# Kernel optimization log

Hardware: AMD Instinct MI355X
Metric: run time of the kernel (lower is better)

## Reference

```python
import jax, jax.numpy as jnp
import numpy as np

EMBED_DIM = 1024
NUM_HEADS = 16
HEAD_DIM = EMBED_DIM // NUM_HEADS


def setup_inputs() -> dict:
    key = jax.random.key(0)
    ks = jax.random.split(key, 11)
    L, N, E = 2048, 2, EMBED_DIM
    S = 2048
    def xavier(k, shape):
        fan_in, fan_out = shape[1], shape[0]
        limit = float(np.sqrt(6.0 / (fan_in + fan_out)))
        return jax.random.uniform(k, shape, jnp.float32, -limit, limit)
    return {
        "query": jax.random.normal(ks[0], (L, N, E), jnp.float32),
        "key": jax.random.normal(ks[1], (S, N, E), jnp.float32),
        "value": jax.random.normal(ks[2], (S, N, E), jnp.float32),
        "Wq": xavier(ks[3], (E, E)), "bq": jnp.zeros((E,), jnp.float32),
        "Wk": xavier(ks[4], (E, E)), "bk": jnp.zeros((E,), jnp.float32),
        "Wv": xavier(ks[5], (E, E)), "bv": jnp.zeros((E,), jnp.float32),
        "Wo": xavier(ks[6], (E, E)), "bo": jnp.zeros((E,), jnp.float32),
    }


def reference(query, key, value, Wq, bq, Wk, bk, Wv, bv, Wo, bo):
    # query/key/value: [L, N, E] (seq-first, batch_first=False)
    L, N, E = query.shape
    S = key.shape[0]
    H, D = NUM_HEADS, HEAD_DIM
    q = query @ Wq.T + bq   # [L, N, E]
    k = key @ Wk.T + bk     # [S, N, E]
    v = value @ Wv.T + bv   # [S, N, E]
    # [L, N*H, D] -> [N*H, L, D]
    q = q.reshape(L, N * H, D).transpose(1, 0, 2)
    k = k.reshape(S, N * H, D).transpose(1, 0, 2)
    v = v.reshape(S, N * H, D).transpose(1, 0, 2)
    scores = jnp.einsum("bld,bsd->bls", q, k) / jnp.sqrt(jnp.float32(D))  # [N*H, L, S]
    attn = jax.nn.softmax(scores, axis=-1)  # dropout p=0.0 -> identity
    out = jnp.einsum("bls,bsd->bld", attn, v)  # [N*H, L, D]
    out = out.transpose(1, 0, 2).reshape(L, N, E)
    attn_output = out @ Wo.T + bo  # [L, N, E]
    # need_weights=True, average_attn_weights=True
    attn_weights = attn.reshape(N, H, L, S).mean(axis=1)  # [N, L, S]
    return attn_output, attn_weights
```

## Files before the change

kernel.cpp:

```cpp
#include <hip/hip_runtime.h>

#define EDIM 1024
#define LSEQ 2048
#define NBATCH 2
#define NHEADS 16
#define HDIM 64
#define QSCALE 0.18033688011112042f

typedef unsigned short us;
typedef __attribute__((ext_vector_type(8))) short short8;
typedef __attribute__((ext_vector_type(4))) float floatx4;
typedef __attribute__((ext_vector_type(16))) float floatx16;

#define MFMA16(a, b, c) __builtin_amdgcn_mfma_f32_16x16x32_bf16((a), (b), (c), 0, 0, 0)
#define MFMA32(a, b, c) __builtin_amdgcn_mfma_f32_32x32x16_bf16((a), (b), (c), 0, 0, 0)
#define ZERO16 ((floatx16){0.f,0.f,0.f,0.f,0.f,0.f,0.f,0.f,0.f,0.f,0.f,0.f,0.f,0.f,0.f,0.f})

#define WAIT_VM8 asm volatile("s_waitcnt vmcnt(8)" ::: "memory")
#define WAIT_VM4 asm volatile("s_waitcnt vmcnt(4)" ::: "memory")
#define WAIT_VM0 asm volatile("s_waitcnt vmcnt(0)" ::: "memory")
#define WAIT_LGKM0 asm volatile("s_waitcnt lgkmcnt(0)" ::: "memory")
#define CFENCE asm volatile("" ::: "memory")

__device__ __forceinline__ us f2bf(float f) {
  unsigned int u = __float_as_uint(f);
  u += 0x7fffu + ((u >> 16) & 1u);
  return (us)(u >> 16);
}

__device__ __forceinline__ void gload16(const void* g, void* l) {
  __builtin_amdgcn_global_load_lds((const __attribute__((address_space(1))) unsigned int*)g,
                                   (__attribute__((address_space(3))) unsigned int*)l, 16, 0, 0);
}

__device__ __forceinline__ unsigned int cvtpk(float lo, float hi_) {
  unsigned int r;
  asm("v_cvt_pk_bf16_f32 %0, %1, %2" : "=v"(r) : "v"(lo), "v"(hi_));
  return r;
}
__device__ __forceinline__ void plswap(unsigned int& a, unsigned int& b) {
  asm("v_permlane32_swap_b32 %0, %1" : "+v"(a), "+v"(b));
}
__device__ __forceinline__ short8 mkfrag(unsigned int a, unsigned int b, unsigned int c,
                                         unsigned int d) {
  union { unsigned int u[4]; short8 v; } x;
  x.u[0] = a; x.u[1] = b; x.u[2] = c; x.u[3] = d;
  return x.v;
}
__device__ __forceinline__ void pack2(const floatx16 p, short8& f0, short8& f1) {
  unsigned int A = cvtpk(p[0], p[1]), B = cvtpk(p[4], p[5]); plswap(A, B);
  unsigned int C = cvtpk(p[2], p[3]), D = cvtpk(p[6], p[7]); plswap(C, D);
  f0 = mkfrag(A, C, B, D);
  unsigned int E = cvtpk(p[8], p[9]), F = cvtpk(p[12], p[13]); plswap(E, F);
  unsigned int G = cvtpk(p[10], p[11]), H = cvtpk(p[14], p[15]); plswap(G, H);
  f1 = mkfrag(E, G, F, H);
}

__global__ void k_f2bf_all(const float* q, const float* k, const float* v,
                           const float* wq, const float* wk, const float* wv, const float* wo,
                           us* dq, us* dk, us* dv, us* dwq, us* dwk, us* dwv, us* dwo) {
  const int z = blockIdx.y;
  const float* s; us* d; int n8;
  if (z == 0)      { s = q;  d = dq;  n8 = 524288; }
  else if (z == 1) { s = k;  d = dk;  n8 = 524288; }
  else if (z == 2) { s = v;  d = dv;  n8 = 524288; }
  else if (z == 3) { s = wq; d = dwq; n8 = 131072; }
  else if (z == 4) { s = wk; d = dwk; n8 = 131072; }
  else if (z == 5) { s = wv; d = dwv; n8 = 131072; }
  else             { s = wo; d = dwo; n8 = 131072; }
  int i = blockIdx.x * blockDim.x + threadIdx.x;
  int stride = gridDim.x * blockDim.x;
  for (; i < n8; i += stride) {
    float4 a = ((const float4*)s)[2 * i];
    float4 b = ((const float4*)s)[2 * i + 1];
    union { us u[8]; uint4 vv; } o;
    o.u[0] = f2bf(a.x); o.u[1] = f2bf(a.y); o.u[2] = f2bf(a.z); o.u[3] = f2bf(a.w);
    o.u[4] = f2bf(b.x); o.u[5] = f2bf(b.y); o.u[6] = f2bf(b.z); o.u[7] = f2bf(b.w);
    ((uint4*)d)[i] = o.vv;
  }
}

template <int MODE>
__device__ __forceinline__ void gemm_core(us* pool,
                                          const us* __restrict__ A, const us* __restrict__ B,
                                          const float* __restrict__ bias, void* __restrict__ outp,
                                          int row0, int col0, float scale) {
  const int t = threadIdx.x;
  const int w = t >> 6, lane = t & 63;
  const int g = lane >> 4, lr = lane & 15;
  const int wm = (w & 1) * 64, wn = (w >> 1) * 64;
  const int srow = lane >> 2, scol = (lane & 3) * 8;
  const int cA = 2 * w;
  const us* Asrc = A + (size_t)(row0 + cA * 16 + srow) * EDIM + scol;
  const us* Bsrc = B + (size_t)(col0 + cA * 16 + srow) * EDIM + scol;

  floatx4 acc[4][4];
#pragma unroll
  for (int mi = 0; mi < 4; ++mi)
#pragma unroll
    for (int ni = 0; ni < 4; ++ni) acc[mi][ni] = (floatx4){0.f, 0.f, 0.f, 0.f};

  auto stage = [&](int kt, us* Ab) {
    const int k0 = kt * 32;
    us* Bb = Ab + 4096;
    gload16(Asrc + k0, Ab + cA * 512);
    gload16(Asrc + 16 * EDIM + k0, Ab + cA * 512 + 512);
    gload16(Bsrc + k0, Bb + cA * 512);
    gload16(Bsrc + 16 * EDIM + k0, Bb + cA * 512 + 512);
  };

  stage(0, pool);
  stage(1, pool + 8192);

  int cur = 0, nxt = 2;
  for (int kt = 0; kt < 32; ++kt) {
    if (kt < 31) { WAIT_VM4; } else { WAIT_VM0; }
    __builtin_amdgcn_s_barrier();
    CFENCE;
    if (kt + 2 < 32) {
      stage(kt + 2, pool + nxt * 8192);
      nxt = (nxt == 2) ? 0 : nxt + 1;
    }
    const us* Ac = pool + cur * 8192;
    const us* Bc = Ac + 4096;
    short8 af[4], bfr[4];
#pragma unroll
    for (int mi = 0; mi < 4; ++mi) af[mi] = *(const short8*)&Ac[(wm + mi * 16 + lr) * 32 + g * 8];
#pragma unroll
    for (int ni = 0; ni < 4; ++ni) bfr[ni] = *(const short8*)&Bc[(wn + ni * 16 + lr) * 32 + g * 8];
#pragma unroll
    for (int mi = 0; mi < 4; ++mi)
#pragma unroll
      for (int ni = 0; ni < 4; ++ni) acc[mi][ni] = MFMA16(af[mi], bfr[ni], acc[mi][ni]);
    WAIT_LGKM0;
    CFENCE;
    cur = (cur == 2) ? 0 : cur + 1;
  }

  if (MODE == 1) {
    __syncthreads();
    us* Ct = pool;
#pragma unroll
    for (int ni = 0; ni < 4; ++ni) {
      const int colloc = wn + ni * 16 + lr;
      const float bv = bias[col0 + colloc];
#pragma unroll
      for (int mi = 0; mi < 4; ++mi) {
        const int b = wm + mi * 16 + 4 * g;
        unsigned int lo = (unsigned int)f2bf(acc[mi][ni][0] + bv) |
                          ((unsigned int)f2bf(acc[mi][ni][2] + bv) << 16);
        unsigned int hi = (unsigned int)f2bf(acc[mi][ni][1] + bv) |
                          ((unsigned int)f2bf(acc[mi][ni][3] + bv) << 16);
        *(unsigned int*)&Ct[colloc * 136 + (b >> 1)] = lo;
        *(unsigned int*)&Ct[colloc * 136 + 64 + (b >> 1)] = hi;
      }
    }
    __syncthreads();
    const int rr = t >> 1, half = t & 1;
    const int c = col0 + rr, h = c >> 6, d = c & 63;
    us* dst = (us*)outp + (((size_t)half * NHEADS + h) * HDIM + d) * LSEQ + (row0 >> 1);
    const us* srcRow = &Ct[rr * 136 + half * 64];
#pragma unroll
    for (int j = 0; j < 8; ++j)
      *(uint4*)(dst + j * 8) = *(const uint4*)(srcRow + j * 8);
  } else {
#pragma unroll
    for (int ni = 0; ni < 4; ++ni) {
      const int col = col0 + wn + ni * 16 + lr;
      const float bv = bias[col];
#pragma unroll
      for (int mi = 0; mi < 4; ++mi) {
#pragma unroll
        for (int i = 0; i < 4; ++i) {
          const int row = row0 + wm + mi * 16 + g * 4 + i;
          const float v = (acc[mi][ni][i] + bv) * scale;
          if (MODE == 2) {
            ((float*)outp)[(size_t)row * EDIM + col] = v;
          } else {
            const int n = row & 1, sq = row >> 1;
            const int h = col >> 6, d = col & 63;
            ((us*)outp)[(((size_t)n * NHEADS + h) * LSEQ + sq) * HDIM + d] = f2bf(v);
          }
        }
      }
    }
  }
}

__global__ __launch_bounds__(256) void k_gemm_qkv(
    const us* __restrict__ Xq, const us* __restrict__ Xk, const us* __restrict__ Xv,
    const us* __restrict__ Wqb, const us* __restrict__ Wkb, const us* __restrict__ Wvb,
    const float* __restrict__ bq, const float* __restrict__ bk, const float* __restrict__ bv,
    us* __restrict__ qo, us* __restrict__ ko, us* __restrict__ vo) {
  __shared__ us pool[24576];
  const int z = blockIdx.z;
  if (z == 0)      gemm_core<0>(pool, Xq, Wqb, bq, qo, blockIdx.x * 128, blockIdx.y * 128, QSCALE);
  else if (z == 1) gemm_core<0>(pool, Xk, Wkb, bk, ko, blockIdx.x * 128, blockIdx.y * 128, 1.0f);
  else             gemm_core<1>(pool, Xv, Wvb, bv, vo, blockIdx.x * 128, blockIdx.y * 128, 1.0f);
}

__global__ __launch_bounds__(256) void k_gemm_o(const us* __restrict__ A, const us* __restrict__ B,
                                                const float* __restrict__ bias, float* __restrict__ out) {
  __shared__ us pool[24576];
  gemm_core<2>(pool, A, B, bias, out, blockIdx.x * 128, blockIdx.y * 128, 1.0f);
}

__global__ __launch_bounds__(256) void k_attn(const us* __restrict__ qb, const us* __restrict__ kb,
                                              const us* __restrict__ vt, float* __restrict__ rell,
                                              us* __restrict__ O) {
  __shared__ us Ks[4][4096];
  __shared__ us Vs[4][4096];
  __shared__ float elt[4][32];
  const int bh = blockIdx.x;
  const int l0 = blockIdx.y * 128;
  const int t = threadIdx.x, w = t >> 6, lane = t & 63;
  const int ql = lane & 31, hi = lane >> 5;
  const int lbase = l0 + w * 32;

  short8 qf[4];
  {
    const us* qptr = qb + ((size_t)bh * LSEQ + lbase + ql) * HDIM + hi * 8;
#pragma unroll
    for (int dt = 0; dt < 4; ++dt) qf[dt] = *(const short8*)(qptr + dt * 16);
  }

  int off0[4], off1[4];
#pragma unroll
  for (int j = 0; j < 4; ++j) {
    off0[j] = ql * 64 + (((2 * j + hi) ^ (ql & 7)) << 3);
    off1[j] = (32 + ql) * 64 + (((2 * j + hi) ^ (ql & 7)) << 3);
  }

  const int j0 = 2 * w, j1 = 2 * w + 1;
  const int srA = lane >> 3;
  const int scA = ((lane & 7) ^ (lane >> 3)) * 8;
  const us* Kbase = kb + (size_t)bh * LSEQ * HDIM;
  const us* Vbase = vt + (size_t)bh * HDIM * LSEQ;
  const us* Ksrc0 = Kbase + (j0 * 8 + srA) * HDIM + scA;
  const us* Ksrc1 = Kbase + (j1 * 8 + srA) * HDIM + scA;
  const us* Vsrc0 = Vbase + (size_t)(j0 * 8 + srA) * LSEQ + scA;
  const us* Vsrc1 = Vbase + (size_t)(j1 * 8 + srA) * LSEQ + scA;

  floatx16 oacc0 = ZERO16, oacc1 = ZERO16;
  float ellacc = 0.f;

  auto stageKV = [&](int kt, int b) {
    const int so = kt * 64;
    gload16(Ksrc0 + so * HDIM, &Ks[b][j0 * 512]);
    gload16(Ksrc1 + so * HDIM, &Ks[b][j1 * 512]);
    gload16(Vsrc0 + so, &Vs[b][j0 * 512]);
    gload16(Vsrc1 + so, &Vs[b][j1 * 512]);
  };

  stageKV(0, 0);
  stageKV(1, 1);
  stageKV(2, 2);

  for (int it = 0; it < 32; ++it) {
    if (it < 30) { WAIT_VM8; } else if (it == 30) { WAIT_VM4; } else { WAIT_VM0; }
    __builtin_amdgcn_s_barrier();
    CFENCE;
    if (it + 3 < 32) stageKV(it + 3, (it + 3) & 3);
    const us* Kc = Ks[it & 3];
    const us* Vc = Vs[it & 3];

    floatx16 acc0 = ZERO16, acc1 = ZERO16;
    __builtin_amdgcn_s_setprio(1);
#pragma unroll
    for (int dt = 0; dt < 4; ++dt) {
      acc0 = MFMA32(*(const short8*)&Kc[off0[dt]], qf[dt], acc0);
      acc1 = MFMA32(*(const short8*)&Kc[off1[dt]], qf[dt], acc1);
    }
    __builtin_amdgcn_s_setprio(0);
#pragma unroll
    for (int r = 0; r < 16; ++r) {
      acc0[r] = __builtin_amdgcn_exp2f(acc0[r]); ellacc += acc0[r];
      acc1[r] = __builtin_amdgcn_exp2f(acc1[r]); ellacc += acc1[r];
    }
    short8 pa0, pa1, pa2, pa3;
    pack2(acc0, pa0, pa1);
    pack2(acc1, pa2, pa3);
    __builtin_amdgcn_s_setprio(1);
#pragma unroll
    for (int dt2 = 0; dt2 < 2; ++dt2) {
      floatx16& oa = dt2 ? oacc1 : oacc0;
      const int* off = dt2 ? off1 : off0;
      oa = MFMA32(pa0, *(const short8*)&Vc[off[0]], oa);
      oa = MFMA32(pa1, *(const short8*)&Vc[off[1]], oa);
      oa = MFMA32(pa2, *(const short8*)&Vc[off[2]], oa);
      oa = MFMA32(pa3, *(const short8*)&Vc[off[3]], oa);
    }
    __builtin_amdgcn_s_setprio(0);
  }

  const float elltot = ellacc + __shfl_xor(ellacc, 32);
  if (lane < 32) {
    const float r0 = 1.0f / elltot;
    elt[w][lane] = r0;
    rell[(size_t)bh * LSEQ + lbase + lane] = r0;
  }
  const int n = bh >> 4, hh = bh & 15;
  us* obase = O + (size_t)n * EDIM + (size_t)hh * HDIM;
#pragma unroll
  for (int r = 0; r < 16; ++r) {
    const int q = (r & 3) + 8 * (r >> 2) + 4 * hi;
    const float rl = elt[w][q];
    const size_t l = lbase + q;
    obase[l * (NBATCH * EDIM) + ql] = f2bf(oacc0[r] * rl);
    obase[l * (NBATCH * EDIM) + 32 + ql] = f2bf(oacc1[r] * rl);
  }
}

__global__ __launch_bounds__(256, 2) void k_weights(const us* __restrict__ qb, const us* __restrict__ kb,
                                                    const float* __restrict__ rell,
                                                    float* __restrict__ Wout) {
  __shared__ us Ks[2][4096];
  const int l0 = blockIdx.x * 256;
  const int s0 = blockIdx.y * 64;
  const int n = blockIdx.z;
  const int t = threadIdx.x, w = t >> 6, lane = t & 63;
  const int ql = lane & 31, hi = lane >> 5;
  const int lbase = l0 + w * 64;
  const int j0 = 2 * w, j1 = 2 * w + 1;
  const int srA = lane >> 3;
  const int scA = ((lane & 7) ^ (lane >> 3)) * 8;
  const us* Kb0 = kb + ((size_t)(n * NHEADS) * LSEQ + s0 + j0 * 8 + srA) * HDIM + scA;
  const us* Kb1 = kb + ((size_t)(n * NHEADS) * LSEQ + s0 + j1 * 8 + srA) * HDIM + scA;

  int off0[4], off1[4];
#pragma unroll
  for (int j = 0; j < 4; ++j) {
    off0[j] = ql * 64 + (((2 * j + hi) ^ (ql & 7)) << 3);
    off1[j] = (32 + ql) * 64 + (((2 * j + hi) ^ (ql & 7)) << 3);
  }

  floatx16 wa00 = ZERO16, wa01 = ZERO16, wa10 = ZERO16, wa11 = ZERO16;

  gload16(Kb0, &Ks[0][j0 * 512]); gload16(Kb1, &Ks[0][j1 * 512]);

  short8 qc0[4], qc1[4];
  float rlc0, rlc1;
  {
    const us* qp0 = qb + ((size_t)(n * NHEADS) * LSEQ + lbase + ql) * HDIM + hi * 8;
    const us* qp1 = qp0 + 32 * HDIM;
#pragma unroll
    for (int dt = 0; dt < 4; ++dt) {
      qc0[dt] = *(const short8*)(qp0 + dt * 16);
      qc1[dt] = *(const short8*)(qp1 + dt * 16);
    }
    rlc0 = rell[(size_t)(n * NHEADS) * LSEQ + lbase + ql];
    rlc1 = rell[(size_t)(n * NHEADS) * LSEQ + lbase + 32 + ql];
  }
  __syncthreads();

  for (int h = 0; h < NHEADS; ++h) {
    const int cur = h & 1;
    short8 qn0[4], qn1[4];
    float rln0 = 0.f, rln1 = 0.f;
    if (h < NHEADS - 1) {
      us* Kn2 = Ks[cur ^ 1];
      gload16(Kb0 + (size_t)(h + 1) * LSEQ * HDIM, Kn2 + j0 * 512);
      gload16(Kb1 + (size_t)(h + 1) * LSEQ * HDIM, Kn2 + j1 * 512);
      const us* qp0 = qb + ((size_t)(n * NHEADS + h + 1) * LSEQ + lbase + ql) * HDIM + hi * 8;
      const us* qp1 = qp0 + 32 * HDIM;
#pragma unroll
      for (int dt = 0; dt < 4; ++dt) {
        qn0[dt] = *(const short8*)(qp0 + dt * 16);
        qn1[dt] = *(const short8*)(qp1 + dt * 16);
      }
      rln0 = rell[(size_t)(n * NHEADS + h + 1) * LSEQ + lbase + ql];
      rln1 = rell[(size_t)(n * NHEADS + h + 1) * LSEQ + lbase + 32 + ql];
    }
    const us* Kc = Ks[cur];
    short8 kf0[4], kf1[4];
#pragma unroll
    for (int dt = 0; dt < 4; ++dt) {
      kf0[dt] = *(const short8*)&Kc[off0[dt]];
      kf1[dt] = *(const short8*)&Kc[off1[dt]];
    }
    {
      floatx16 aA = ZERO16, aB = ZERO16;
#pragma unroll
      for (int dt = 0; dt < 4; ++dt) {
        aA = MFMA32(kf0[dt], qc0[dt], aA);
        aB = MFMA32(kf1[dt], qc0[dt], aB);
      }
#pragma unroll
      for (int r = 0; r < 16; ++r) {
        wa00[r] += __builtin_amdgcn_exp2f(aA[r]) * rlc0;
        wa01[r] += __builtin_amdgcn_exp2f(aB[r]) * rlc0;
      }
    }
    {
      floatx16 cA = ZERO16, cB = ZERO16;
#pragma unroll
      for (int dt = 0; dt < 4; ++dt) {
        cA = MFMA32(kf0[dt], qc1[dt], cA);
        cB = MFMA32(kf1[dt], qc1[dt], cB);
      }
#pragma unroll
      for (int r = 0; r < 16; ++r) {
        wa10[r] += __builtin_amdgcn_exp2f(cA[r]) * rlc1;
        wa11[r] += __builtin_amdgcn_exp2f(cB[r]) * rlc1;
      }
    }
#pragma unroll
    for (int dt = 0; dt < 4; ++dt) { qc0[dt] = qn0[dt]; qc1[dt] = qn1[dt]; }
    rlc0 = rln0; rlc1 = rln1;
    __syncthreads();
  }

  float* wb0 = Wout + (size_t)n * LSEQ * LSEQ + (size_t)(lbase + ql) * LSEQ + s0;
  float* wb1 = Wout + (size_t)n * LSEQ * LSEQ + (size_t)(lbase + 32 + ql) * LSEQ + s0;
#pragma unroll
  for (int r = 0; r < 16; ++r) {
    const int cr = (r & 3) + 8 * (r >> 2) + 4 * hi;
    wb0[cr] = wa00[r] * 0.0625f;
    wb0[32 + cr] = wa01[r] * 0.0625f;
    wb1[cr] = wa10[r] * 0.0625f;
    wb1[32 + cr] = wa11[r] * 0.0625f;
  }
}

extern "C" void kernel_launch(void* const* d_in, const int* in_sizes, int n_in,
                              void* d_out, int out_size, void* d_ws, size_t ws_size,
                              hipStream_t stream) {
  const float* query = (const float*)d_in[0];
  const float* key   = (const float*)d_in[1];
  const float* value = (const float*)d_in[2];
  const float* Wq = (const float*)d_in[3]; const float* bq = (const float*)d_in[4];
  const float* Wk = (const float*)d_in[5]; const float* bk = (const float*)d_in[6];
  const float* Wv = (const float*)d_in[7]; const float* bv = (const float*)d_in[8];
  const float* Wo = (const float*)d_in[9]; const float* bo = (const float*)d_in[10];

  const size_t MB = 1u << 20;
  char* ws = (char*)d_ws;
  us* Xq  = (us*)(ws + 0 * MB);
  us* Xk  = (us*)(ws + 8 * MB);
  us* Xv  = (us*)(ws + 16 * MB);
  us* Wqb = (us*)(ws + 24 * MB);
  us* Wkb = (us*)(ws + 26 * MB);
  us* Wvb = (us*)(ws + 28 * MB);
  us* Wob = (us*)(ws + 30 * MB);
  us* qbuf = (us*)(ws + 32 * MB);
  us* kbuf = (us*)(ws + 40 * MB);
  us* Vt   = (us*)(ws + 48 * MB);
  us* Obuf = (us*)(ws + 56 * MB);
  float* rell = (float*)(ws + 64 * MB);

  k_f2bf_all<<<dim3(256, 7), 256, 0, stream>>>(query, key, value, Wq, Wk, Wv, Wo,
                                               Xq, Xk, Xv, Wqb, Wkb, Wvb, Wob);

  k_gemm_qkv<<<dim3(32, 8, 3), 256, 0, stream>>>(Xq, Xk, Xv, Wqb, Wkb, Wvb, bq, bk, bv,
                                                 qbuf, kbuf, Vt);

  k_attn<<<dim3(32, 16), 256, 0, stream>>>(qbuf, kbuf, Vt, rell, Obuf);

  k_gemm_o<<<dim3(32, 8), 256, 0, stream>>>(Obuf, Wob, bo, (float*)d_out);
  k_weights<<<dim3(8, 32, 2), 256, 0, stream>>>(qbuf, kbuf, rell, (float*)d_out + 4194304);
}
```

Measured before the change: 156.7 us.

## Merge output projection GEMM and attention-weights kernels into one interleaved launch

Combines the output-projection GEMM (256 blocks) and the averaged attention-weights kernel (512 blocks) into a single 768-block launch. Block ids are interleaved so every third block runs the GEMM and the rest compute weights. The aim is to remove one launch and the tail idle time between the two kernels, letting the independent pieces of work fill the device together. In exchange the GEMM now runs under launch_bounds(256,2) with the larger shared pool, which may constrain its registers or occupancy.

```diff
diff --git a/kernel.cpp b/kernel.cpp
--- a/kernel.cpp
+++ b/kernel.cpp
@@ -199,10 +199,132 @@
   else             gemm_core<1>(pool, Xv, Wvb, bv, vo, blockIdx.x * 128, blockIdx.y * 128, 1.0f);
 }
 
-__global__ __launch_bounds__(256) void k_gemm_o(const us* __restrict__ A, const us* __restrict__ B,
-                                                const float* __restrict__ bias, float* __restrict__ out) {
+__device__ __forceinline__ void weights_core(us* poolraw, const us* __restrict__ qb,
+                                             const us* __restrict__ kb,
+                                             const float* __restrict__ rell,
+                                             float* __restrict__ Wout,
+                                             int l0, int s0, int n) {
+  us (*Ks)[4096] = (us(*)[4096])poolraw;
+  const int t = threadIdx.x, w = t >> 6, lane = t & 63;
+  const int ql = lane & 31, hi = lane >> 5;
+  const int lbase = l0 + w * 64;
+  const int j0 = 2 * w, j1 = 2 * w + 1;
+  const int srA = lane >> 3;
+  const int scA = ((lane & 7) ^ (lane >> 3)) * 8;
+  const us* Kb0 = kb + ((size_t)(n * NHEADS) * LSEQ + s0 + j0 * 8 + srA) * HDIM + scA;
+  const us* Kb1 = kb + ((size_t)(n * NHEADS) * LSEQ + s0 + j1 * 8 + srA) * HDIM + scA;
+
+  int off0[4], off1[4];
+#pragma unroll
+  for (int j = 0; j < 4; ++j) {
+    off0[j] = ql * 64 + (((2 * j + hi) ^ (ql & 7)) << 3);
+    off1[j] = (32 + ql) * 64 + (((2 * j + hi) ^ (ql & 7)) << 3);
+  }
+
+  floatx16 wa00 = ZERO16, wa01 = ZERO16, wa10 = ZERO16, wa11 = ZERO16;
+
+  gload16(Kb0, &Ks[0][j0 * 512]); gload16(Kb1, &Ks[0][j1 * 512]);
+
+  short8 qc0[4], qc1[4];
+  float rlc0, rlc1;
+  {
+    const us* qp0 = qb + ((size_t)(n * NHEADS) * LSEQ + lbase + ql) * HDIM + hi * 8;
+    const us* qp1 = qp0 + 32 * HDIM;
+#pragma unroll
+    for (int dt = 0; dt < 4; ++dt) {
+      qc0[dt] = *(const short8*)(qp0 + dt * 16);
+      qc1[dt] = *(const short8*)(qp1 + dt * 16);
+    }
+    rlc0 = rell[(size_t)(n * NHEADS) * LSEQ + lbase + ql];
+    rlc1 = rell[(size_t)(n * NHEADS) * LSEQ + lbase + 32 + ql];
+  }
+  __syncthreads();
+
+  for (int h = 0; h < NHEADS; ++h) {
+    const int cur = h & 1;
+    short8 qn0[4], qn1[4];
+    float rln0 = 0.f, rln1 = 0.f;
+    if (h < NHEADS - 1) {
+      us* Kn2 = Ks[cur ^ 1];
+      gload16(Kb0 + (size_t)(h + 1) * LSEQ * HDIM, Kn2 + j0 * 512);
+      gload16(Kb1 + (size_t)(h + 1) * LSEQ * HDIM, Kn2 + j1 * 512);
+      const us* qp0 = qb + ((size_t)(n * NHEADS + h + 1) * LSEQ + lbase + ql) * HDIM + hi * 8;
+      const us* qp1 = qp0 + 32 * HDIM;
+#pragma unroll
+      for (int dt = 0; dt < 4; ++dt) {
+        qn0[dt] = *(const short8*)(qp0 + dt * 16);
+        qn1[dt] = *(const short8*)(qp1 + dt * 16);
+      }
+      rln0 = rell[(size_t)(n * NHEADS + h + 1) * LSEQ + lbase + ql];
+      rln1 = rell[(size_t)(n * NHEADS + h + 1) * LSEQ + lbase + 32 + ql];
+    }
+    const us* Kc = Ks[cur];
+    short8 kf0[4], kf1[4];
+#pragma unroll
+    for (int dt = 0; dt < 4; ++dt) {
+      kf0[dt] = *(const short8*)&Kc[off0[dt]];
+      kf1[dt] = *(const short8*)&Kc[off1[dt]];
+    }
+    {
+      floatx16 aA = ZERO16, aB = ZERO16;
+#pragma unroll
+      for (int dt = 0; dt < 4; ++dt) {
+        aA = MFMA32(kf0[dt], qc0[dt], aA);
+        aB = MFMA32(kf1[dt], qc0[dt], aB);
+      }
+#pragma unroll
+      for (int r = 0; r < 16; ++r) {
+        wa00[r] += __builtin_amdgcn_exp2f(aA[r]) * rlc0;
+        wa01[r] += __builtin_amdgcn_exp2f(aB[r]) * rlc0;
+      }
+    }
+    {
+      floatx16 cA = ZERO16, cB = ZERO16;
+#pragma unroll
+      for (int dt = 0; dt < 4; ++dt) {
+        cA = MFMA32(kf0[dt], qc1[dt], cA);
+        cB = MFMA32(kf1[dt], qc1[dt], cB);
+      }
+#pragma unroll
+      for (int r = 0; r < 16; ++r) {
+        wa10[r] += __builtin_amdgcn_exp2f(cA[r]) * rlc1;
+        wa11[r] += __builtin_amdgcn_exp2f(cB[r]) * rlc1;
+      }
+    }
+#pragma unroll
+    for (int dt = 0; dt < 4; ++dt) { qc0[dt] = qn0[dt]; qc1[dt] = qn1[dt]; }
+    rlc0 = rln0; rlc1 = rln1;
+    __syncthreads();
+  }
+
+  float* wb0 = Wout + (size_t)n * LSEQ * LSEQ + (size_t)(lbase + ql) * LSEQ + s0;
+  float* wb1 = Wout + (size_t)n * LSEQ * LSEQ + (size_t)(lbase + 32 + ql) * LSEQ + s0;
+#pragma unroll
+  for (int r = 0; r < 16; ++r) {
+    const int cr = (r & 3) + 8 * (r >> 2) + 4 * hi;
+    wb0[cr] = wa00[r] * 0.0625f;
+    wb0[32 + cr] = wa01[r] * 0.0625f;
+    wb1[cr] = wa10[r] * 0.0625f;
+    wb1[32 + cr] = wa11[r] * 0.0625f;
+  }
+}
+
+__global__ __launch_bounds__(256, 2) void k_tail(
+    const us* __restrict__ Obuf, const us* __restrict__ Wob, const float* __restrict__ bo,
+    float* __restrict__ out, const us* __restrict__ qb, const us* __restrict__ kb,
+    const float* __restrict__ rell, float* __restrict__ Wout) {
   __shared__ us pool[24576];
-  gemm_core<2>(pool, A, B, bias, out, blockIdx.x * 128, blockIdx.y * 128, 1.0f);
+  const int id = blockIdx.x;
+  if (id % 3 == 0) {
+    const int gid = id / 3;
+    gemm_core<2>(pool, Obuf, Wob, bo, out, (gid & 31) * 128, (gid >> 5) * 128, 1.0f);
+  } else {
+    const int wid = id - id / 3 - 1;
+    const int l0 = (wid & 7) * 256;
+    const int s0 = ((wid >> 3) & 31) * 64;
+    const int n = wid >> 8;
+    weights_core(pool, qb, kb, rell, Wout, l0, s0, n);
+  }
 }
 
 __global__ __launch_bounds__(256) void k_attn(const us* __restrict__ qb, const us* __restrict__ kb,
@@ -308,117 +430,6 @@
     const size_t l = lbase + q;
     obase[l * (NBATCH * EDIM) + ql] = f2bf(oacc0[r] * rl);
     obase[l * (NBATCH * EDIM) + 32 + ql] = f2bf(oacc1[r] * rl);
-  }
-}
-
-__global__ __launch_bounds__(256, 2) void k_weights(const us* __restrict__ qb, const us* __restrict__ kb,
-                                                    const float* __restrict__ rell,
-                                                    float* __restrict__ Wout) {
-  __shared__ us Ks[2][4096];
-  const int l0 = blockIdx.x * 256;
-  const int s0 = blockIdx.y * 64;
-  const int n = blockIdx.z;
-  const int t = threadIdx.x, w = t >> 6, lane = t & 63;
-  const int ql = lane & 31, hi = lane >> 5;
-  const int lbase = l0 + w * 64;
-  const int j0 = 2 * w, j1 = 2 * w + 1;
-  const int srA = lane >> 3;
-  const int scA = ((lane & 7) ^ (lane >> 3)) * 8;
-  const us* Kb0 = kb + ((size_t)(n * NHEADS) * LSEQ + s0 + j0 * 8 + srA) * HDIM + scA;
-  const us* Kb1 = kb + ((size_t)(n * NHEADS) * LSEQ + s0 + j1 * 8 + srA) * HDIM + scA;
-
-  int off0[4], off1[4];
-#pragma unroll
-  for (int j = 0; j < 4; ++j) {
-    off0[j] = ql * 64 + (((2 * j + hi) ^ (ql & 7)) << 3);
-    off1[j] = (32 + ql) * 64 + (((2 * j + hi) ^ (ql & 7)) << 3);
-  }
-
-  floatx16 wa00 = ZERO16, wa01 = ZERO16, wa10 = ZERO16, wa11 = ZERO16;
-
-  gload16(Kb0, &Ks[0][j0 * 512]); gload16(Kb1, &Ks[0][j1 * 512]);
-
-  short8 qc0[4], qc1[4];
-  float rlc0, rlc1;
-  {
-    const us* qp0 = qb + ((size_t)(n * NHEADS) * LSEQ + lbase + ql) * HDIM + hi * 8;
-    const us* qp1 = qp0 + 32 * HDIM;
-#pragma unroll
-    for (int dt = 0; dt < 4; ++dt) {
-      qc0[dt] = *(const short8*)(qp0 + dt * 16);
-      qc1[dt] = *(const short8*)(qp1 + dt * 16);
-    }
-    rlc0 = rell[(size_t)(n * NHEADS) * LSEQ + lbase + ql];
-    rlc1 = rell[(size_t)(n * NHEADS) * LSEQ + lbase + 32 + ql];
-  }
-  __syncthreads();
-
-  for (int h = 0; h < NHEADS; ++h) {
-    const int cur = h & 1;
-    short8 qn0[4], qn1[4];
-    float rln0 = 0.f, rln1 = 0.f;
-    if (h < NHEADS - 1) {
-      us* Kn2 = Ks[cur ^ 1];
-      gload16(Kb0 + (size_t)(h + 1) * LSEQ * HDIM, Kn2 + j0 * 512);
-      gload16(Kb1 + (size_t)(h + 1) * LSEQ * HDIM, Kn2 + j1 * 512);
-      const us* qp0 = qb + ((size_t)(n * NHEADS + h + 1) * LSEQ + lbase + ql) * HDIM + hi * 8;
-      const us* qp1 = qp0 + 32 * HDIM;
-#pragma unroll
-      for (int dt = 0; dt < 4; ++dt) {
-        qn0[dt] = *(const short8*)(qp0 + dt * 16);
-        qn1[dt] = *(const short8*)(qp1 + dt * 16);
-      }
-      rln0 = rell[(size_t)(n * NHEADS + h + 1) * LSEQ + lbase + ql];
-      rln1 = rell[(size_t)(n * NHEADS + h + 1) * LSEQ + lbase + 32 + ql];
-    }
-    const us* Kc = Ks[cur];
-    short8 kf0[4], kf1[4];
-#pragma unroll
-    for (int dt = 0; dt < 4; ++dt) {
-      kf0[dt] = *(const short8*)&Kc[off0[dt]];
-      kf1[dt] = *(const short8*)&Kc[off1[dt]];
-    }
-    {
-      floatx16 aA = ZERO16, aB = ZERO16;
-#pragma unroll
-      for (int dt = 0; dt < 4; ++dt) {
-        aA = MFMA32(kf0[dt], qc0[dt], aA);
-        aB = MFMA32(kf1[dt], qc0[dt], aB);
-      }
-#pragma unroll
-      for (int r = 0; r < 16; ++r) {
-        wa00[r] += __builtin_amdgcn_exp2f(aA[r]) * rlc0;
-        wa01[r] += __builtin_amdgcn_exp2f(aB[r]) * rlc0;
-      }
-    }
-    {
-      floatx16 cA = ZERO16, cB = ZERO16;
-#pragma unroll
-      for (int dt = 0; dt < 4; ++dt) {
-        cA = MFMA32(kf0[dt], qc1[dt], cA);
-        cB = MFMA32(kf1[dt], qc1[dt], cB);
-      }
-#pragma unroll
-      for (int r = 0; r < 16; ++r) {
-        wa10[r] += __builtin_amdgcn_exp2f(cA[r]) * rlc1;
-        wa11[r] += __builtin_amdgcn_exp2f(cB[r]) * rlc1;
-      }
-    }
-#pragma unroll
-    for (int dt = 0; dt < 4; ++dt) { qc0[dt] = qn0[dt]; qc1[dt] = qn1[dt]; }
-    rlc0 = rln0; rlc1 = rln1;
-    __syncthreads();
-  }
-
-  float* wb0 = Wout + (size_t)n * LSEQ * LSEQ + (size_t)(lbase + ql) * LSEQ + s0;
-  float* wb1 = Wout + (size_t)n * LSEQ * LSEQ + (size_t)(lbase + 32 + ql) * LSEQ + s0;
-#pragma unroll
-  for (int r = 0; r < 16; ++r) {
-    const int cr = (r & 3) + 8 * (r >> 2) + 4 * hi;
-    wb0[cr] = wa00[r] * 0.0625f;
-    wb0[32 + cr] = wa01[r] * 0.0625f;
-    wb1[cr] = wa10[r] * 0.0625f;
-    wb1[32 + cr] = wa11[r] * 0.0625f;
   }
 }
 
@@ -456,6 +467,6 @@
 
   k_attn<<<dim3(32, 16), 256, 0, stream>>>(qbuf, kbuf, Vt, rell, Obuf);
 
-  k_gemm_o<<<dim3(32, 8), 256, 0, stream>>>(Obuf, Wob, bo, (float*)d_out);
-  k_weights<<<dim3(8, 32, 2), 256, 0, stream>>>(qbuf, kbuf, rell, (float*)d_out + 4194304);
-}
+  k_tail<<<dim3(768), 256, 0, stream>>>(Obuf, Wob, bo, (float*)d_out,
+                                        qbuf, kbuf, rell, (float*)d_out + 4194304);
+}
```

Measured after the change: 166.5 us. 6.3% more time.

## Give each attention wave 64 query rows to reuse K/V fragments across two tiles

Applied to the files above, without the earlier changes.

The attention kernel now runs 2 waves of 128 threads per block instead of 4. Each wave handles 64 query rows as two 32-row tiles that share the K and V fragments loaded from LDS, and each thread issues twice as many async global-to-LDS loads, with the vmcnt waits adjusted to match. This halves the LDS reads of K/V per unit of MFMA work and gives each wave more independent MFMA chains. In exchange it raises register pressure from four output accumulators and fewer waves per block, which may lower occupancy and latency hiding.

```diff
diff --git a/kernel.cpp b/kernel.cpp
--- a/kernel.cpp
+++ b/kernel.cpp
@@ -16,6 +16,7 @@
 #define MFMA32(a, b, c) __builtin_amdgcn_mfma_f32_32x32x16_bf16((a), (b), (c), 0, 0, 0)
 #define ZERO16 ((floatx16){0.f,0.f,0.f,0.f,0.f,0.f,0.f,0.f,0.f,0.f,0.f,0.f,0.f,0.f,0.f,0.f})
 
+#define WAIT_VM16 asm volatile("s_waitcnt vmcnt(16)" ::: "memory")
 #define WAIT_VM8 asm volatile("s_waitcnt vmcnt(8)" ::: "memory")
 #define WAIT_VM4 asm volatile("s_waitcnt vmcnt(4)" ::: "memory")
 #define WAIT_VM0 asm volatile("s_waitcnt vmcnt(0)" ::: "memory")
@@ -205,23 +206,27 @@
   gemm_core<2>(pool, A, B, bias, out, blockIdx.x * 128, blockIdx.y * 128, 1.0f);
 }
 
-__global__ __launch_bounds__(256) void k_attn(const us* __restrict__ qb, const us* __restrict__ kb,
+__global__ __launch_bounds__(128) void k_attn(const us* __restrict__ qb, const us* __restrict__ kb,
                                               const us* __restrict__ vt, float* __restrict__ rell,
                                               us* __restrict__ O) {
   __shared__ us Ks[4][4096];
   __shared__ us Vs[4][4096];
-  __shared__ float elt[4][32];
+  __shared__ float elt[2][64];
   const int bh = blockIdx.x;
   const int l0 = blockIdx.y * 128;
   const int t = threadIdx.x, w = t >> 6, lane = t & 63;
   const int ql = lane & 31, hi = lane >> 5;
-  const int lbase = l0 + w * 32;
-
-  short8 qf[4];
+  const int lbase = l0 + w * 64;
+
+  short8 qfA[4], qfB[4];
   {
-    const us* qptr = qb + ((size_t)bh * LSEQ + lbase + ql) * HDIM + hi * 8;
-#pragma unroll
-    for (int dt = 0; dt < 4; ++dt) qf[dt] = *(const short8*)(qptr + dt * 16);
+    const us* qpA = qb + ((size_t)bh * LSEQ + lbase + ql) * HDIM + hi * 8;
+    const us* qpB = qpA + 32 * HDIM;
+#pragma unroll
+    for (int dt = 0; dt < 4; ++dt) {
+      qfA[dt] = *(const short8*)(qpA + dt * 16);
+      qfB[dt] = *(const short8*)(qpB + dt * 16);
+    }
   }
 
   int off0[4], off1[4];
@@ -231,25 +236,29 @@
     off1[j] = (32 + ql) * 64 + (((2 * j + hi) ^ (ql & 7)) << 3);
   }
 
-  const int j0 = 2 * w, j1 = 2 * w + 1;
   const int srA = lane >> 3;
   const int scA = ((lane & 7) ^ (lane >> 3)) * 8;
   const us* Kbase = kb + (size_t)bh * LSEQ * HDIM;
   const us* Vbase = vt + (size_t)bh * HDIM * LSEQ;
-  const us* Ksrc0 = Kbase + (j0 * 8 + srA) * HDIM + scA;
-  const us* Ksrc1 = Kbase + (j1 * 8 + srA) * HDIM + scA;
-  const us* Vsrc0 = Vbase + (size_t)(j0 * 8 + srA) * LSEQ + scA;
-  const us* Vsrc1 = Vbase + (size_t)(j1 * 8 + srA) * LSEQ + scA;
-
-  floatx16 oacc0 = ZERO16, oacc1 = ZERO16;
-  float ellacc = 0.f;
+  const us* Ksrc[4];
+  const us* Vsrc[4];
+#pragma unroll
+  for (int i = 0; i < 4; ++i) {
+    const int jj = 4 * w + i;
+    Ksrc[i] = Kbase + (jj * 8 + srA) * HDIM + scA;
+    Vsrc[i] = Vbase + (size_t)(jj * 8 + srA) * LSEQ + scA;
+  }
+
+  floatx16 oaA0 = ZERO16, oaA1 = ZERO16, oaB0 = ZERO16, oaB1 = ZERO16;
+  float ellA = 0.f, ellB = 0.f;
 
   auto stageKV = [&](int kt, int b) {
     const int so = kt * 64;
-    gload16(Ksrc0 + so * HDIM, &Ks[b][j0 * 512]);
-    gload16(Ksrc1 + so * HDIM, &Ks[b][j1 * 512]);
-    gload16(Vsrc0 + so, &Vs[b][j0 * 512]);
-    gload16(Vsrc1 + so, &Vs[b][j1 * 512]);
+#pragma unroll
+    for (int i = 0; i < 4; ++i) {
+      gload16(Ksrc[i] + so * HDIM, &Ks[b][(4 * w + i) * 512]);
+      gload16(Vsrc[i] + so, &Vs[b][(4 * w + i) * 512]);
+    }
   };
 
   stageKV(0, 0);
@@ -257,57 +266,94 @@
   stageKV(2, 2);
 
   for (int it = 0; it < 32; ++it) {
-    if (it < 30) { WAIT_VM8; } else if (it == 30) { WAIT_VM4; } else { WAIT_VM0; }
+    if (it < 30) { WAIT_VM16; } else if (it == 30) { WAIT_VM8; } else { WAIT_VM0; }
     __builtin_amdgcn_s_barrier();
     CFENCE;
     if (it + 3 < 32) stageKV(it + 3, (it + 3) & 3);
     const us* Kc = Ks[it & 3];
     const us* Vc = Vs[it & 3];
 
-    floatx16 acc0 = ZERO16, acc1 = ZERO16;
+    short8 kf0[4], kf1[4];
+#pragma unroll
+    for (int dt = 0; dt < 4; ++dt) {
+      kf0[dt] = *(const short8*)&Kc[off0[dt]];
+      kf1[dt] = *(const short8*)&Kc[off1[dt]];
+    }
+    short8 paA[4];
+    {
+      floatx16 a0 = ZERO16, a1 = ZERO16;
+      __builtin_amdgcn_s_setprio(1);
+#pragma unroll
+      for (int dt = 0; dt < 4; ++dt) {
+        a0 = MFMA32(kf0[dt], qfA[dt], a0);
+        a1 = MFMA32(kf1[dt], qfA[dt], a1);
+      }
+      __builtin_amdgcn_s_setprio(0);
+#pragma unroll
+      for (int r = 0; r < 16; ++r) {
+        a0[r] = __builtin_amdgcn_exp2f(a0[r]); ellA += a0[r];
+        a1[r] = __builtin_amdgcn_exp2f(a1[r]); ellA += a1[r];
+      }
+      pack2(a0, paA[0], paA[1]);
+      pack2(a1, paA[2], paA[3]);
+    }
+    short8 paB[4];
+    {
+      floatx16 c0 = ZERO16, c1 = ZERO16;
+      __builtin_amdgcn_s_setprio(1);
+#pragma unroll
+      for (int dt = 0; dt < 4; ++dt) {
+        c0 = MFMA32(kf0[dt], qfB[dt], c0);
+        c1 = MFMA32(kf1[dt], qfB[dt], c1);
+      }
+      __builtin_amdgcn_s_setprio(0);
+#pragma unroll
+      for (int r = 0; r < 16; ++r) {
+        c0[r] = __builtin_amdgcn_exp2f(c0[r]); ellB += c0[r];
+        c1[r] = __builtin_amdgcn_exp2f(c1[r]); ellB += c1[r];
+      }
+      pack2(c0, paB[0], paB[1]);
+      pack2(c1, paB[2], paB[3]);
+    }
     __builtin_amdgcn_s_setprio(1);
 #pragma unroll
-    for (int dt = 0; dt < 4; ++dt) {
-      acc0 = MFMA32(*(const short8*)&Kc[off0[dt]], qf[dt], acc0);
-      acc1 = MFMA32(*(const short8*)&Kc[off1[dt]], qf[dt], acc1);
+    for (int j = 0; j < 4; ++j) {
+      const short8 vf0 = *(const short8*)&Vc[off0[j]];
+      const short8 vf1 = *(const short8*)&Vc[off1[j]];
+      oaA0 = MFMA32(paA[j], vf0, oaA0);
+      oaA1 = MFMA32(paA[j], vf1, oaA1);
+      oaB0 = MFMA32(paB[j], vf0, oaB0);
+      oaB1 = MFMA32(paB[j], vf1, oaB1);
     }
     __builtin_amdgcn_s_setprio(0);
-#pragma unroll
-    for (int r = 0; r < 16; ++r) {
-      acc0[r] = __builtin_amdgcn_exp2f(acc0[r]); ellacc += acc0[r];
-      acc1[r] = __builtin_amdgcn_exp2f(acc1[r]); ellacc += acc1[r];
-    }
-    short8 pa0, pa1, pa2, pa3;
-    pack2(acc0, pa0, pa1);
-    pack2(acc1, pa2, pa3);
-    __builtin_amdgcn_s_setprio(1);
-#pragma unroll
-    for (int dt2 = 0; dt2 < 2; ++dt2) {
-      floatx16& oa = dt2 ? oacc1 : oacc0;
-      const int* off = dt2 ? off1 : off0;
-      oa = MFMA32(pa0, *(const short8*)&Vc[off[0]], oa);
-      oa = MFMA32(pa1, *(const short8*)&Vc[off[1]], oa);
-      oa = MFMA32(pa2, *(const short8*)&Vc[off[2]], oa);
-      oa = MFMA32(pa3, *(const short8*)&Vc[off[3]], oa);
-    }
-    __builtin_amdgcn_s_setprio(0);
-  }
-
-  const float elltot = ellacc + __shfl_xor(ellacc, 32);
+  }
+
+  const float eA = ellA + __shfl_xor(ellA, 32);
+  const float eB = ellB + __shfl_xor(ellB, 32);
   if (lane < 32) {
-    const float r0 = 1.0f / elltot;
-    elt[w][lane] = r0;
-    rell[(size_t)bh * LSEQ + lbase + lane] = r0;
+    const float rA = 1.0f / eA, rB = 1.0f / eB;
+    elt[w][lane] = rA;
+    elt[w][32 + lane] = rB;
+    rell[(size_t)bh * LSEQ + lbase + lane] = rA;
+    rell[(size_t)bh * LSEQ + lbase + 32 + lane] = rB;
   }
   const int n = bh >> 4, hh = bh & 15;
   us* obase = O + (size_t)n * EDIM + (size_t)hh * HDIM;
 #pragma unroll
   for (int r = 0; r < 16; ++r) {
     const int q = (r & 3) + 8 * (r >> 2) + 4 * hi;
-    const float rl = elt[w][q];
-    const size_t l = lbase + q;
-    obase[l * (NBATCH * EDIM) + ql] = f2bf(oacc0[r] * rl);
-    obase[l * (NBATCH * EDIM) + 32 + ql] = f2bf(oacc1[r] * rl);
+    {
+      const float rl = elt[w][q];
+      const size_t l = lbase + q;
+      obase[l * (NBATCH * EDIM) + ql] = f2bf(oaA0[r] * rl);
+      obase[l * (NBATCH * EDIM) + 32 + ql] = f2bf(oaA1[r] * rl);
+    }
+    {
+      const float rl = elt[w][32 + q];
+      const size_t l = lbase + 32 + q;
+      obase[l * (NBATCH * EDIM) + ql] = f2bf(oaB0[r] * rl);
+      obase[l * (NBATCH * EDIM) + 32 + ql] = f2bf(oaB1[r] * rl);
+    }
   }
 }
 
@@ -454,7 +500,7 @@
   k_gemm_qkv<<<dim3(32, 8, 3), 256, 0, stream>>>(Xq, Xk, Xv, Wqb, Wkb, Wvb, bq, bk, bv,
                                                  qbuf, kbuf, Vt);
 
-  k_attn<<<dim3(32, 16), 256, 0, stream>>>(qbuf, kbuf, Vt, rell, Obuf);
+  k_attn<<<dim3(32, 16), 128, 0, stream>>>(qbuf, kbuf, Vt, rell, Obuf);
 
   k_gemm_o<<<dim3(32, 8), 256, 0, stream>>>(Obuf, Wob, bo, (float*)d_out);
   k_weights<<<dim3(8, 32, 2), 256, 0, stream>>>(qbuf, kbuf, rell, (float*)d_out + 4194304);
```

Result: slower. 174.1 us (+11.1%).
